# Optimization experiments

Measured on AMD Instinct MI355X. Metric: run time of the kernel, lower is better.

## Reference

```python
import jax, jax.numpy as jnp
import numpy as np
import math

BS, LQ, LKV = 4, 2048, 2048
D_LATENT, D_MODEL, HEADS = 512, 512, 8
D_K = D_MODEL // HEADS


def setup_inputs() -> dict:
    key = jax.random.key(0)
    ks = jax.random.split(key, 12)
    s = 0.02
    return {
        "q": jax.random.normal(ks[0], (BS, LQ, D_LATENT), jnp.float32),
        "k": jax.random.normal(ks[1], (BS, LKV, D_MODEL), jnp.float32),
        "v": jax.random.normal(ks[2], (BS, LKV, D_MODEL), jnp.float32),
        "weights": jax.random.uniform(ks[3], (BS, LKV), jnp.float32) + 1e-3,
        "Wq": jax.random.normal(ks[4], (D_LATENT, D_MODEL), jnp.float32) * s,
        "bq": jnp.zeros((D_MODEL,), jnp.float32),
        "Wk": jax.random.normal(ks[5], (D_MODEL, D_MODEL), jnp.float32) * s,
        "bk": jnp.zeros((D_MODEL,), jnp.float32),
        "Wv": jax.random.normal(ks[6], (D_MODEL, D_MODEL), jnp.float32) * s,
        "bv": jnp.zeros((D_MODEL,), jnp.float32),
        "Wo": jax.random.normal(ks[7], (D_MODEL, D_MODEL), jnp.float32) * s,
        "bo": jnp.zeros((D_MODEL,), jnp.float32),
    }


def reference(q, k, v, weights, Wq, bq, Wk, bk, Wv, bv, Wo, bo):
    bs = q.shape[0]
    # QKV projections, split into heads: [bs, h, L, d_k]
    qh = (q @ Wq + bq).reshape(bs, -1, HEADS, D_K).transpose(0, 2, 1, 3)
    kh = (k @ Wk + bk).reshape(bs, -1, HEADS, D_K).transpose(0, 2, 1, 3)
    vh = (v @ Wv + bv).reshape(bs, -1, HEADS, D_K).transpose(0, 2, 1, 3)
    # scaled dot-product scores [bs, h, Lq, Lkv]
    scores = jnp.einsum("bhqd,bhkd->bhqk", qh, kh) / math.sqrt(D_K)
    p = jax.nn.softmax(scores, axis=-1)
    # post-softmax external weight renormalization
    wp = p * weights[:, None, None, :]
    wp = wp / wp.sum(-1, keepdims=True)
    out = jnp.einsum("bhqk,bhkd->bhqd", wp, vh)
    concat = out.transpose(0, 2, 1, 3).reshape(bs, -1, D_MODEL)
    return concat @ Wo + bo
```

## Files before the change

kernel.cpp:

```cpp
#include <hip/hip_runtime.h>
#include <hip/hip_bf16.h>

#define LQ 2048
#define LKV 2048
#define DM 512
#define NH 8
#define DK 64

typedef __attribute__((ext_vector_type(8))) __bf16 bf16x8;
typedef __attribute__((ext_vector_type(4))) float f32x4;
typedef __attribute__((ext_vector_type(16))) float f32x16;

#define AS1 __attribute__((address_space(1)))
#define AS3 __attribute__((address_space(3)))

static __device__ __forceinline__ unsigned short f2bf(float x) {
  unsigned u = __float_as_uint(x);
  return (unsigned short)((u + 0x7fffu + ((u >> 16) & 1u)) >> 16);
}
static __device__ __forceinline__ float bf2f(unsigned short u) {
  return __uint_as_float(((unsigned)u) << 16);
}
static __device__ __forceinline__ bf16x8 cvt8(f32x4 a, f32x4 b) {
  bf16x8 r;
  r[0] = (__bf16)a[0]; r[1] = (__bf16)a[1]; r[2] = (__bf16)a[2]; r[3] = (__bf16)a[3];
  r[4] = (__bf16)b[0]; r[5] = (__bf16)b[1]; r[6] = (__bf16)b[2]; r[7] = (__bf16)b[3];
  return r;
}

__global__ __launch_bounds__(256) void transpose_w(
    const float* __restrict__ Wq, const float* __restrict__ Wk,
    const float* __restrict__ Wv, const float* __restrict__ Wo,
    unsigned short* __restrict__ WtAll)
{
  const float* W = blockIdx.z == 0 ? Wq : blockIdx.z == 1 ? Wk : blockIdx.z == 2 ? Wv : Wo;
  unsigned short* Wt = WtAll + (size_t)blockIdx.z * DM * DM;
  __shared__ float tile[32][33];
  const int t = threadIdx.x;
  const int tr = t >> 3;
  const int tc4 = (t & 7) * 4;
  const int k0 = blockIdx.x * 32, n0 = blockIdx.y * 32;
  float4 v = *(const float4*)(W + (size_t)(k0 + tr) * DM + n0 + tc4);
  tile[tr][tc4 + 0] = v.x; tile[tr][tc4 + 1] = v.y;
  tile[tr][tc4 + 2] = v.z; tile[tr][tc4 + 3] = v.w;
  __syncthreads();
  ushort4 o;
  o.x = f2bf(tile[tc4 + 0][tr]);
  o.y = f2bf(tile[tc4 + 1][tr]);
  o.z = f2bf(tile[tc4 + 2][tr]);
  o.w = f2bf(tile[tc4 + 3][tr]);
  *(ushort4*)(Wt + (size_t)(n0 + tr) * DM + k0 + tc4) = o;
}

__global__ __launch_bounds__(256) void gemm_qkv(
    const float* __restrict__ qin, const float* __restrict__ kin, const float* __restrict__ vin,
    const unsigned short* __restrict__ WtAll,
    const float* __restrict__ bq, const float* __restrict__ bk, const float* __restrict__ bv,
    unsigned short* __restrict__ qh, unsigned short* __restrict__ kh, unsigned short* __restrict__ vh)
{
  const int bid = blockIdx.x;
  const int x = bid & 7, j = bid >> 3;
  const int p = x + 8 * (j >> 2);
  const int nt = j & 3;
  const int mode = p >> 6, mtile = p & 63;

  const float* A = mode == 0 ? qin : (mode == 1 ? kin : vin);
  const unsigned short* Bt = WtAll + (size_t)mode * DM * DM;
  const float* bias = mode == 0 ? bq : (mode == 1 ? bk : bv);
  unsigned short* out = mode == 0 ? qh : (mode == 1 ? kh : vh);
  const float scale = (mode == 0) ? 0.18033688011112042f : 1.0f;

  __shared__ __align__(16) float As[128 * 32];
  __shared__ __align__(16) unsigned short Bs[128 * 32];

  const int tid = threadIdx.x;
  const int lane = tid & 63;
  const int w = tid >> 6;
  const int wr = w >> 1, wc = w & 1;
  const int l15 = lane & 15, g = lane >> 4;
  const int m0 = mtile * 128, n0 = nt * 128;

  f32x4 acc[4][4] = {};

  for (int k0 = 0; k0 < DM; k0 += 32) {
#pragma unroll
    for (int i = 0; i < 4; ++i) {
      int c = tid + i * 256;
      int row = c >> 3, slot = c & 7;
      const float* src = A + (size_t)(m0 + row) * DM + k0 + ((slot ^ (row & 7)) << 2);
      __builtin_amdgcn_global_load_lds((const AS1 unsigned*)src,
                                       (AS3 unsigned*)((char*)As + c * 16), 16, 0, 0);
    }
#pragma unroll
    for (int i = 0; i < 2; ++i) {
      int c = tid + i * 256;
      int row = c >> 2, slot = c & 3;
      const unsigned short* src = Bt + (size_t)(n0 + row) * DM + k0 + ((slot ^ ((row >> 1) & 3)) * 8);
      __builtin_amdgcn_global_load_lds((const AS1 unsigned*)src,
                                       (AS3 unsigned*)((char*)Bs + c * 16), 16, 0, 0);
    }
    __syncthreads();

    bf16x8 af[4], bfr[4];
#pragma unroll
    for (int mi = 0; mi < 4; ++mi) {
      int row = wr * 64 + mi * 16 + l15;
      f32x4 a0 = *(const f32x4*)((const char*)As + row * 128 + (((2 * g) ^ (row & 7)) << 4));
      f32x4 a1 = *(const f32x4*)((const char*)As + row * 128 + (((2 * g + 1) ^ (row & 7)) << 4));
      af[mi] = cvt8(a0, a1);
    }
#pragma unroll
    for (int ni = 0; ni < 4; ++ni) {
      int row = wc * 64 + ni * 16 + l15;
      bfr[ni] = *(const bf16x8*)((const char*)Bs + row * 64 + ((g ^ ((row >> 1) & 3)) * 16));
    }
#pragma unroll
    for (int mi = 0; mi < 4; ++mi)
#pragma unroll
      for (int ni = 0; ni < 4; ++ni)
        acc[mi][ni] = __builtin_amdgcn_mfma_f32_16x16x32_bf16(af[mi], bfr[ni], acc[mi][ni], 0, 0, 0);
    __syncthreads();
  }

#pragma unroll
  for (int mi = 0; mi < 4; ++mi) {
#pragma unroll
    for (int ni = 0; ni < 4; ++ni) {
      int n = n0 + wc * 64 + ni * 16 + l15;
      float bs = bias[n];
      int h = n >> 6, d = n & 63;
#pragma unroll
      for (int r = 0; r < 4; ++r) {
        int m = m0 + wr * 64 + mi * 16 + g * 4 + r;
        int b = m >> 11, li = m & 2047;
        float val = (acc[mi][ni][r] + bs) * scale;
        out[(((size_t)(b * NH + h)) * LQ + li) * DK + d] = f2bf(val);
      }
    }
  }
}

__global__ __launch_bounds__(256) void gemm_out(
    const unsigned short* __restrict__ A, const unsigned short* __restrict__ Bt,
    const float* __restrict__ bias, float* __restrict__ out)
{
  __shared__ __align__(16) unsigned short Al[128 * 40];
  __shared__ __align__(16) unsigned short Bl[128 * 40];
  const int tid = threadIdx.x;
  const int lane = tid & 63;
  const int w = tid >> 6;
  const int wr = w >> 1, wc = w & 1;
  const int l15 = lane & 15, g = lane >> 4;
  const int m0 = blockIdx.x * 128, n0 = blockIdx.y * 128;
  f32x4 acc[4][4] = {};

  for (int k0 = 0; k0 < DM; k0 += 32) {
#pragma unroll
    for (int i = 0; i < 2; ++i) {
      int idx = tid + i * 256;
      int row = idx >> 2, seg = idx & 3;
      *(int4*)(&Al[row * 40 + seg * 8]) =
          *(const int4*)(A + (size_t)(m0 + row) * DM + k0 + seg * 8);
      *(int4*)(&Bl[row * 40 + seg * 8]) =
          *(const int4*)(Bt + (size_t)(n0 + row) * DM + k0 + seg * 8);
    }
    __syncthreads();
    bf16x8 af[4], bfr[4];
#pragma unroll
    for (int mi = 0; mi < 4; ++mi)
      af[mi] = *(const bf16x8*)(&Al[(wr * 64 + mi * 16 + l15) * 40 + g * 8]);
#pragma unroll
    for (int ni = 0; ni < 4; ++ni)
      bfr[ni] = *(const bf16x8*)(&Bl[(wc * 64 + ni * 16 + l15) * 40 + g * 8]);
#pragma unroll
    for (int mi = 0; mi < 4; ++mi)
#pragma unroll
      for (int ni = 0; ni < 4; ++ni)
        acc[mi][ni] = __builtin_amdgcn_mfma_f32_16x16x32_bf16(af[mi], bfr[ni], acc[mi][ni], 0, 0, 0);
    __syncthreads();
  }

#pragma unroll
  for (int mi = 0; mi < 4; ++mi) {
#pragma unroll
    for (int ni = 0; ni < 4; ++ni) {
      int n = n0 + wc * 64 + ni * 16 + l15;
      float bs = bias[n];
#pragma unroll
      for (int r = 0; r < 4; ++r) {
        int m = m0 + wr * 64 + mi * 16 + g * 4 + r;
        out[(size_t)m * DM + n] = acc[mi][ni][r] + bs;
      }
    }
  }
}

__global__ __launch_bounds__(256) void prep_kv(
    const unsigned short* __restrict__ kh, const unsigned short* __restrict__ vh,
    const float* __restrict__ wts,
    unsigned short* __restrict__ kf, unsigned short* __restrict__ vf,
    unsigned short* __restrict__ wbf)
{
  __shared__ __align__(16) unsigned short t[64 * 72];
  const int bh = blockIdx.y, l0 = blockIdx.x * 64;
  const int b = bh >> 3;
  const size_t base = (size_t)bh * LKV * DK;
  const int tid = threadIdx.x;

  if ((bh & 7) == 0 && tid < 64)
    wbf[b * LKV + l0 + tid] = f2bf(wts[b * LKV + l0 + tid]);

#pragma unroll
  for (int i = 0; i < 2; ++i) {
    int c = tid + i * 256;
    int sl = c & 63, cq = (c >> 6) & 3, tl = c >> 8;
    int kv = tl * 32 + (sl & 31);
    int4 blk = *(const int4*)(kh + base + (size_t)(l0 + kv) * DK + cq * 16 + (sl >> 5) * 8);
    *(int4*)(kf + base + ((((size_t)(l0 >> 5) + tl) * 4 + cq) * 64 + sl) * 8) = blk;
  }

#pragma unroll
  for (int i = 0; i < 2; ++i) {
    int idx = tid + i * 256;
    int row = idx >> 3, seg = idx & 7;
    *(int4*)(&t[row * 72 + seg * 8]) =
        *(const int4*)(vh + base + (size_t)(l0 + row) * DK + seg * 8);
  }
  __syncthreads();
#pragma unroll
  for (int i = 0; i < 2; ++i) {
    int idx = tid + i * 256;
    int d = idx >> 3, seg = idx & 7;
    int kvg = l0 + seg * 8;
    float4 wa = *(const float4*)(wts + b * LKV + kvg);
    float4 wb = *(const float4*)(wts + b * LKV + kvg + 4);
    unsigned short r0 = f2bf(wa.x * bf2f(t[(seg * 8 + 0) * 72 + d]));
    unsigned short r1 = f2bf(wa.y * bf2f(t[(seg * 8 + 1) * 72 + d]));
    unsigned short r2 = f2bf(wa.z * bf2f(t[(seg * 8 + 2) * 72 + d]));
    unsigned short r3 = f2bf(wa.w * bf2f(t[(seg * 8 + 3) * 72 + d]));
    unsigned short r4 = f2bf(wb.x * bf2f(t[(seg * 8 + 4) * 72 + d]));
    unsigned short r5 = f2bf(wb.y * bf2f(t[(seg * 8 + 5) * 72 + d]));
    unsigned short r6 = f2bf(wb.z * bf2f(t[(seg * 8 + 6) * 72 + d]));
    unsigned short r7 = f2bf(wb.w * bf2f(t[(seg * 8 + 7) * 72 + d]));
    int4 o;
    o.x = (int)((unsigned)r0 | ((unsigned)r1 << 16));
    o.y = (int)((unsigned)r2 | ((unsigned)r3 << 16));
    o.z = (int)((unsigned)r4 | ((unsigned)r5 << 16));
    o.w = (int)((unsigned)r6 | ((unsigned)r7 << 16));
    size_t addr = ((((size_t)bh * 128 + (kvg >> 4)) * 2 + (d >> 5)) * 64 +
                   ((d & 31) + ((kvg >> 3) & 1) * 32)) * 8;
    *(int4*)(vf + addr) = o;
  }
}

__global__ __launch_bounds__(512, 4) void attn_fwd(
    const unsigned short* __restrict__ qh, const unsigned short* __restrict__ kf,
    const unsigned short* __restrict__ vf, const unsigned short* __restrict__ wbf,
    unsigned short* __restrict__ ao)
{
  const int bid = blockIdx.x;
  const int xcd = bid & 7, wi = bid >> 3;
  const int bh = xcd * 4 + (wi >> 4);
  const int qb = wi & 15;
  const int b = bh >> 3, h = bh & 7;
  const int tid = threadIdx.x, lane = tid & 63, w = tid >> 6;
  const int wq = w & 3, half = w >> 2;
  const int l31 = lane & 31, hi = lane >> 5;

  __shared__ __align__(16) char smem[35840];

  const size_t kv_bh = (size_t)bh * (LKV * DK);
  const unsigned short* kfb = kf + kv_bh;
  const unsigned short* vfb = vf + kv_bh;
  const unsigned short* wrow = wbf + b * LKV + half * 1024;

  const int q0 = qb * 128 + wq * 32;
  bf16x8 qf[4];
  {
    const unsigned short* qp = qh + kv_bh + (size_t)(q0 + l31) * DK + hi * 8;
#pragma unroll
    for (int cq = 0; cq < 4; ++cq) qf[cq] = *(const bf16x8*)(qp + cq * 16);
  }

  f32x16 accO0 = {}, accO1 = {}, accL = {};

#define STAGE(buf, t)                                                                     \
  do {                                                                                    \
    int tg_ = half * 32 + (t);                                                            \
    const unsigned short* ks_ = kfb + ((size_t)(tg_ * 4 + wq) * 64 + lane) * 8;           \
    const unsigned short* vs_ = vfb + ((size_t)((tg_ * 2 + (wq >> 1)) * 2 + (wq & 1)) * 64 + lane) * 8; \
    char* kd_ = smem + (buf) * 16384 + half * 8192 + wq * 1024;                           \
    char* vd_ = smem + (buf) * 16384 + half * 8192 + 4096 + wq * 1024;                    \
    __builtin_amdgcn_global_load_lds((const AS1 unsigned*)ks_, (AS3 unsigned*)kd_, 16, 0, 0); \
    __builtin_amdgcn_global_load_lds((const AS1 unsigned*)vs_, (AS3 unsigned*)vd_, 16, 0, 0); \
  } while (0)

  STAGE(0, 0);
  __syncthreads();

  int cur = 0;
#pragma unroll 2
  for (int t = 0; t < 32; ++t) {
    if (t < 31) STAGE(cur ^ 1, t + 1);

    const char* Kb = smem + cur * 16384 + half * 8192;
    const char* Vb = Kb + 4096;

    f32x16 s = {};
#pragma unroll
    for (int cq = 0; cq < 4; ++cq) {
      bf16x8 kfr = *(const bf16x8*)(Kb + cq * 1024 + lane * 16);
      s = __builtin_amdgcn_mfma_f32_32x32x16_bf16(kfr, qf[cq], s, 0, 0, 0);
    }

    unsigned D[8];
#pragma unroll
    for (int r2 = 0; r2 < 8; ++r2) {
      float lo = __builtin_amdgcn_exp2f(s[2 * r2]);
      float hv = __builtin_amdgcn_exp2f(s[2 * r2 + 1]);
      __bf16 bl = (__bf16)lo, bh2 = (__bf16)hv;
      unsigned short ul = __builtin_bit_cast(unsigned short, bl);
      unsigned short uh = __builtin_bit_cast(unsigned short, bh2);
      D[r2] = (unsigned)ul | ((unsigned)uh << 16);
    }

    const int kvt = t * 32;
#pragma unroll
    for (int c = 0; c < 2; ++c) {
      int base = 4 * c;
      unsigned s0 = hi ? D[base] : D[base + 2];
      unsigned s1 = hi ? D[base + 1] : D[base + 3];
      unsigned X0 = (unsigned)__shfl_xor((int)s0, 32);
      unsigned X1 = (unsigned)__shfl_xor((int)s1, 32);
      union { unsigned u[4]; bf16x8 v; } pa;
      pa.u[0] = hi ? X0 : D[base];
      pa.u[1] = hi ? X1 : D[base + 1];
      pa.u[2] = hi ? D[base + 2] : X0;
      pa.u[3] = hi ? D[base + 3] : X1;

      bf16x8 vb0 = *(const bf16x8*)(Vb + (c * 2 + 0) * 1024 + lane * 16);
      bf16x8 vb1 = *(const bf16x8*)(Vb + (c * 2 + 1) * 1024 + lane * 16);
      bf16x8 wb = {};
      if (l31 == 0) wb = *(const bf16x8*)(wrow + kvt + c * 16 + hi * 8);

      accO0 = __builtin_amdgcn_mfma_f32_32x32x16_bf16(pa.v, vb0, accO0, 0, 0, 0);
      accO1 = __builtin_amdgcn_mfma_f32_32x32x16_bf16(pa.v, vb1, accO1, 0, 0, 0);
      accL  = __builtin_amdgcn_mfma_f32_32x32x16_bf16(pa.v, wb,  accL,  0, 0, 0);
    }
    __syncthreads();
    cur ^= 1;
  }
#undef STAGE

  float* Ob = (float*)smem;
  float* Lb = (float*)(smem + 34816);
  if (half == 1) {
#pragma unroll
    for (int r = 0; r < 16; ++r) {
      int qp_ = (r & 3) + 8 * (r >> 2) + 4 * hi;
      Ob[(wq * 32 + qp_) * 68 + l31] = accO0[r];
      Ob[(wq * 32 + qp_) * 68 + 32 + l31] = accO1[r];
    }
    if (l31 == 0) {
#pragma unroll
      for (int r = 0; r < 16; ++r) {
        int qp_ = (r & 3) + 8 * (r >> 2) + 4 * hi;
        Lb[wq * 32 + qp_] = accL[r];
      }
    }
  }
  __syncthreads();
  if (half == 0) {
#pragma unroll
    for (int r = 0; r < 16; ++r) {
      int qp_ = (r & 3) + 8 * (r >> 2) + 4 * hi;
      float L = __shfl(accL[r], lane & 32) + Lb[wq * 32 + qp_];
      float inv = 1.0f / L;
      float o0 = accO0[r] + Ob[(wq * 32 + qp_) * 68 + l31];
      float o1 = accO1[r] + Ob[(wq * 32 + qp_) * 68 + 32 + l31];
      size_t off = ((size_t)(b * LQ + q0 + qp_)) * DM + h * DK;
      ao[off + l31] = f2bf(o0 * inv);
      ao[off + 32 + l31] = f2bf(o1 * inv);
    }
  }
}

extern "C" void kernel_launch(void* const* d_in, const int* in_sizes, int n_in,
                              void* d_out, int out_size, void* d_ws, size_t ws_size,
                              hipStream_t stream)
{
  const float* q  = (const float*)d_in[0];
  const float* k  = (const float*)d_in[1];
  const float* v  = (const float*)d_in[2];
  const float* wt = (const float*)d_in[3];
  const float* Wq = (const float*)d_in[4];
  const float* bq = (const float*)d_in[5];
  const float* Wk = (const float*)d_in[6];
  const float* bk = (const float*)d_in[7];
  const float* Wv = (const float*)d_in[8];
  const float* bv = (const float*)d_in[9];
  const float* Wo = (const float*)d_in[10];
  const float* bo = (const float*)d_in[11];

  char* ws = (char*)d_ws;
  unsigned short* qh = (unsigned short*)(ws + 0);
  unsigned short* kfr= (unsigned short*)(ws + 8388608);
  unsigned short* vfr= (unsigned short*)(ws + 16777216);
  unsigned short* ao = (unsigned short*)(ws + 25165824);
  unsigned short* Wt = (unsigned short*)(ws + 33554432);
  unsigned short* vh = (unsigned short*)(ws + 35651584);
  unsigned short* wbf= (unsigned short*)(ws + 44040192);
  unsigned short* kh = ao;

  transpose_w<<<dim3(16, 16, 4), 256, 0, stream>>>(Wq, Wk, Wv, Wo, Wt);
  gemm_qkv<<<768, 256, 0, stream>>>(q, k, v, Wt, bq, bk, bv, qh, kh, vh);
  prep_kv<<<dim3(32, 32), 256, 0, stream>>>(kh, vh, wt, kfr, vfr, wbf);
  attn_fwd<<<512, 512, 0, stream>>>(qh, kfr, vfr, wbf, ao);
  gemm_out<<<dim3(64, 4), 256, 0, stream>>>(ao, Wt + 3 * (size_t)DM * DM, bo, (float*)d_out);
}
```

Baseline: 100.2 us.

## Stage Q and weights through LDS and restructure attention loop synchronization

Q tiles and the per-batch weight row are now loaded into shared memory with async global-to-LDS copies, replacing the per-lane global loads. The main loop now waits on explicit vmcnt counters and raw s_barrier instead of __syncthreads. All K, V and weight fragments are read up front each iteration, and the MFMA section is wrapped in s_setprio so loads can overlap compute. The goal is to remove global-load latency inside the loop and cut synchronization cost. In exchange, LDS use grows from 35840 to 53248 bytes, which may lower occupancy, and the hand-written waitcnt and barrier ordering is fragile.

```diff
diff --git a/kernel.cpp b/kernel.cpp
--- a/kernel.cpp
+++ b/kernel.cpp
@@ -267,22 +267,13 @@
   const int wq = w & 3, half = w >> 2;
   const int l31 = lane & 31, hi = lane >> 5;
 
-  __shared__ __align__(16) char smem[35840];
+  __shared__ __align__(16) char smem[53248];
 
   const size_t kv_bh = (size_t)bh * (LKV * DK);
   const unsigned short* kfb = kf + kv_bh;
   const unsigned short* vfb = vf + kv_bh;
-  const unsigned short* wrow = wbf + b * LKV + half * 1024;
 
   const int q0 = qb * 128 + wq * 32;
-  bf16x8 qf[4];
-  {
-    const unsigned short* qp = qh + kv_bh + (size_t)(q0 + l31) * DK + hi * 8;
-#pragma unroll
-    for (int cq = 0; cq < 4; ++cq) qf[cq] = *(const bf16x8*)(qp + cq * 16);
-  }
-
-  f32x16 accO0 = {}, accO1 = {}, accL = {};
 
 #define STAGE(buf, t)                                                                     \
   do {                                                                                    \
@@ -295,23 +286,59 @@
     __builtin_amdgcn_global_load_lds((const AS1 unsigned*)vs_, (AS3 unsigned*)vd_, 16, 0, 0); \
   } while (0)
 
+#pragma unroll
+  for (int i = 0; i < 2; ++i) {
+    int c = tid + i * 512;
+    const unsigned short* qs = qh + kv_bh + (size_t)(qb * 128) * DK + c * 8;
+    __builtin_amdgcn_global_load_lds((const AS1 unsigned*)qs,
+                                     (AS3 unsigned*)(smem + 36864 + c * 16), 16, 0, 0);
+  }
+  if (tid < 256)
+    __builtin_amdgcn_global_load_lds((const AS1 unsigned*)(wbf + b * LKV + tid * 8),
+                                     (AS3 unsigned*)(smem + 32768 + tid * 16), 16, 0, 0);
   STAGE(0, 0);
-  __syncthreads();
-
+  asm volatile("s_waitcnt vmcnt(0)" ::: "memory");
+  __builtin_amdgcn_s_barrier();
+
+  bf16x8 qf[4];
+#pragma unroll
+  for (int cq = 0; cq < 4; ++cq)
+    qf[cq] = *(const bf16x8*)(smem + 36864 + (wq * 32 + l31) * 128 + cq * 32 + hi * 16);
+
+  const char* wl = smem + 32768 + half * 2048;
+  f32x16 accO0 = {}, accO1 = {}, accL = {};
   int cur = 0;
+
 #pragma unroll 2
   for (int t = 0; t < 32; ++t) {
-    if (t < 31) STAGE(cur ^ 1, t + 1);
+    if (t < 31) {
+      STAGE(cur ^ 1, t + 1);
+      asm volatile("s_waitcnt vmcnt(2)" ::: "memory");
+    } else {
+      asm volatile("s_waitcnt vmcnt(0)" ::: "memory");
+    }
+    __builtin_amdgcn_s_barrier();
 
     const char* Kb = smem + cur * 16384 + half * 8192;
     const char* Vb = Kb + 4096;
-
+    bf16x8 kfr[4], vbr[4], wbr[2];
+#pragma unroll
+    for (int cq = 0; cq < 4; ++cq) kfr[cq] = *(const bf16x8*)(Kb + cq * 1024 + lane * 16);
+#pragma unroll
+    for (int j = 0; j < 4; ++j) vbr[j] = *(const bf16x8*)(Vb + j * 1024 + lane * 16);
+    const int kvt = t * 32;
+#pragma unroll
+    for (int c = 0; c < 2; ++c)
+      wbr[c] = *(const bf16x8*)(wl + kvt * 2 + c * 32 + hi * 16);
+
+    __builtin_amdgcn_s_setprio(1);
     f32x16 s = {};
 #pragma unroll
-    for (int cq = 0; cq < 4; ++cq) {
-      bf16x8 kfr = *(const bf16x8*)(Kb + cq * 1024 + lane * 16);
-      s = __builtin_amdgcn_mfma_f32_32x32x16_bf16(kfr, qf[cq], s, 0, 0, 0);
-    }
+    for (int cq = 0; cq < 4; ++cq)
+      s = __builtin_amdgcn_mfma_f32_32x32x16_bf16(kfr[cq], qf[cq], s, 0, 0, 0);
+
+    asm volatile("s_waitcnt lgkmcnt(0)" ::: "memory");
+    __builtin_amdgcn_s_barrier();
 
     unsigned D[8];
 #pragma unroll
@@ -324,7 +351,6 @@
       D[r2] = (unsigned)ul | ((unsigned)uh << 16);
     }
 
-    const int kvt = t * 32;
 #pragma unroll
     for (int c = 0; c < 2; ++c) {
       int base = 4 * c;
@@ -338,16 +364,14 @@
       pa.u[2] = hi ? D[base + 2] : X0;
       pa.u[3] = hi ? D[base + 3] : X1;
 
-      bf16x8 vb0 = *(const bf16x8*)(Vb + (c * 2 + 0) * 1024 + lane * 16);
-      bf16x8 vb1 = *(const bf16x8*)(Vb + (c * 2 + 1) * 1024 + lane * 16);
-      bf16x8 wb = {};
-      if (l31 == 0) wb = *(const bf16x8*)(wrow + kvt + c * 16 + hi * 8);
-
-      accO0 = __builtin_amdgcn_mfma_f32_32x32x16_bf16(pa.v, vb0, accO0, 0, 0, 0);
-      accO1 = __builtin_amdgcn_mfma_f32_32x32x16_bf16(pa.v, vb1, accO1, 0, 0, 0);
+      bf16x8 z = {};
+      bf16x8 wb = (l31 == 0) ? wbr[c] : z;
+
+      accO0 = __builtin_amdgcn_mfma_f32_32x32x16_bf16(pa.v, vbr[c * 2 + 0], accO0, 0, 0, 0);
+      accO1 = __builtin_amdgcn_mfma_f32_32x32x16_bf16(pa.v, vbr[c * 2 + 1], accO1, 0, 0, 0);
       accL  = __builtin_amdgcn_mfma_f32_32x32x16_bf16(pa.v, wb,  accL,  0, 0, 0);
     }
-    __syncthreads();
+    __builtin_amdgcn_s_setprio(0);
     cur ^= 1;
   }
 #undef STAGE
```

Result: slower. 105.3 us (+5.0%).
